# Kernel tuning notes

Hardware: AMD Instinct MI355X
Metric: run time of the kernel (lower is better)

Reference implementation:

```python
import jax, jax.numpy as jnp
import numpy as np

B, N, E = 4, 8192, 131072
NODE_F, EDGE_F, HID, ACT = 16, 1, 128, 8


def _glorot(key, shape):
    fan_in, fan_out = shape[0], shape[1]
    lim = np.sqrt(6.0 / (fan_in + fan_out))
    return jax.random.uniform(key, shape, jnp.float32, -lim, lim)


def setup_inputs() -> dict:
    key = jax.random.key(0)
    ks = jax.random.split(key, 20)
    inp = {
        'node_features': jax.random.randint(ks[0], (B, N, NODE_F), 0, 10, jnp.int32),
        'edge_index': jax.random.randint(ks[1], (B, 2, E), 0, N, jnp.int64),
        'edge_features': jax.random.normal(ks[2], (B, E, EDGE_F), jnp.float32),
        # conv1: in = 2*NODE_F + EDGE_F
        'c1_w1': _glorot(ks[3], (2 * NODE_F + EDGE_F, HID)), 'c1_b1': jnp.zeros((HID,), jnp.float32),
        'c1_w2': _glorot(ks[4], (HID, HID)), 'c1_b2': jnp.zeros((HID,), jnp.float32),
        # conv2/conv3: in = 2*HID + 1
        'c2_w1': _glorot(ks[5], (2 * HID + 1, HID)), 'c2_b1': jnp.zeros((HID,), jnp.float32),
        'c2_w2': _glorot(ks[6], (HID, HID)), 'c2_b2': jnp.zeros((HID,), jnp.float32),
        'c3_w1': _glorot(ks[7], (2 * HID + 1, HID)), 'c3_b1': jnp.zeros((HID,), jnp.float32),
        'c3_w2': _glorot(ks[8], (HID, HID)), 'c3_b2': jnp.zeros((HID,), jnp.float32),
        'lin_w': _glorot(ks[9], (NODE_F + HID, ACT)), 'lin_b': jnp.zeros((ACT,), jnp.float32),
    }
    return inp


def _edge_conv(x, src, dst, ea, w1, b1, w2, b2):
    # message: cat([x_i (target), x_j (source), edge_attr]) -> Linear -> LeakyReLU -> Linear
    m = jnp.concatenate([x[dst], x[src], ea], axis=1)          # [E, 2F+EF]
    m = jax.nn.leaky_relu(m @ w1 + b1) @ w2 + b2               # [E, out]
    out = jax.ops.segment_min(m, dst, num_segments=x.shape[0])  # min-aggregate at targets
    cnt = jnp.zeros((x.shape[0],), m.dtype).at[dst].add(1.0)
    return jnp.where(cnt[:, None] > 0, out, 0.0)                # nodes w/o in-edges -> 0 (PyG)


def _graph_fwd(x0, ei, ea, p):
    x0 = x0.astype(jnp.float32)  # torch casts to IntTensor then MLP promotes; math on integer values
    src, dst = ei[0], ei[1]      # flow='source_to_target'
    x = jax.nn.leaky_relu(_edge_conv(x0, src, dst, ea, p['c1_w1'], p['c1_b1'], p['c1_w2'], p['c1_b2']))
    x = jax.nn.leaky_relu(_edge_conv(x, src, dst, ea, p['c2_w1'], p['c2_b1'], p['c2_w2'], p['c2_b2']))
    x = jax.nn.leaky_relu(_edge_conv(x, src, dst, ea, p['c3_w1'], p['c3_b1'], p['c3_w2'], p['c3_b2']))
    x = jnp.concatenate([x0, x], axis=1)
    return jax.nn.softplus(x @ p['lin_w'] + p['lin_b'])         # [N, ACT]


def reference(node_features, edge_index, edge_features,
              c1_w1, c1_b1, c1_w2, c1_b2,
              c2_w1, c2_b1, c2_w2, c2_b2,
              c3_w1, c3_b1, c3_w2, c3_b2,
              lin_w, lin_b):
    p = dict(c1_w1=c1_w1, c1_b1=c1_b1, c1_w2=c1_w2, c1_b2=c1_b2,
             c2_w1=c2_w1, c2_b1=c2_b1, c2_w2=c2_w2, c2_b2=c2_b2,
             c3_w1=c3_w1, c3_b1=c3_b1, c3_w2=c3_w2, c3_b2=c3_b2,
             lin_w=lin_w, lin_b=lin_b)
    return jax.vmap(lambda x, ei, ea: _graph_fwd(x, ei, ea, p))(
        node_features, edge_index, edge_features)               # [B, N, ACT]
```

## Files before the change

### kernel.cpp

```cpp
#include <hip/hip_runtime.h>

#define B_ 4
#define N_ 8192
#define E_ 131072
#define HID_ 128

typedef unsigned short us8 __attribute__((ext_vector_type(8)));
typedef unsigned short us4 __attribute__((ext_vector_type(4)));
typedef unsigned int   ui4 __attribute__((ext_vector_type(4)));
typedef int            i4  __attribute__((ext_vector_type(4)));
typedef __bf16         v8bf __attribute__((ext_vector_type(8)));
typedef _Float16       hf8 __attribute__((ext_vector_type(8)));
typedef float          v4f  __attribute__((ext_vector_type(4)));
typedef float          v2f  __attribute__((ext_vector_type(2)));

#define KEY_INF 0xFF800000u

__device__ __forceinline__ float b2f(unsigned short u) {
    return __uint_as_float(((unsigned)u) << 16);
}
__device__ __forceinline__ unsigned short f2b(float f) {
    unsigned x = __float_as_uint(f);
    return (unsigned short)((x + 0x7fffu + ((x >> 16) & 1u)) >> 16);
}
__device__ __forceinline__ unsigned short f2h(float f) {
    union { _Float16 h; unsigned short u; } c; c.h = (_Float16)f; return c.u;
}
__device__ __forceinline__ unsigned fkey(float f) {
    unsigned b = __float_as_uint(f);
    return (b & 0x80000000u) ? ~b : (b | 0x80000000u);
}
__device__ __forceinline__ float funkey(unsigned k) {
    unsigned b = (k & 0x80000000u) ? (k ^ 0x80000000u) : ~k;
    return __uint_as_float(b);
}

__device__ __forceinline__ void repack_one(const float* __restrict__ w1, const float* __restrict__ w2,
                                           unsigned short* __restrict__ w1n, unsigned short* __restrict__ w2t,
                                           int F, int KPAD, int gid) {
    int t1 = 256 * KPAD;
    if (gid < t1) {
        int j = gid / KPAD, k = gid - j * KPAD;
        float v = 0.f;
        if (k < F) v = (j < 128) ? w1[k * 128 + j] : w1[(F + k) * 128 + (j - 128)];
        w1n[gid] = f2b(v);
    } else {
        int g = gid - t1;
        if (g < 16384) { int j = g >> 7, k = g & 127; w2t[g] = f2h(w2[k * 128 + j]); }
    }
}

__global__ void k_setup(const int* __restrict__ nf, unsigned short* __restrict__ x0b,
                        unsigned* __restrict__ cnt, unsigned* __restrict__ agg,
                        const float* __restrict__ w1a, const float* __restrict__ w2a,
                        const float* __restrict__ w1b, const float* __restrict__ w2b,
                        const float* __restrict__ w1c, const float* __restrict__ w2c,
                        unsigned short* __restrict__ w1n0, unsigned short* __restrict__ w2t0,
                        unsigned short* __restrict__ w1n1, unsigned short* __restrict__ w2t1,
                        unsigned short* __restrict__ w1n2, unsigned short* __restrict__ w2t2) {
    const int bid = blockIdx.x, tid = threadIdx.x;
    if (bid >= 4096) {
        const int rb = bid - 4096;
        const int gid = rb * 256 + tid;
        if (rb < 96)       repack_one(w1a, w2a, w1n0, w2t0, 16, 32, gid);
        else if (rb < 288) repack_one(w1b, w2b, w1n1, w2t1, 128, 128, gid - 96 * 256);
        else               repack_one(w1c, w2c, w1n2, w2t2, 128, 128, gid - 288 * 256);
        return;
    }
    const int gid = bid * 256 + tid;
    ui4 v = {KEY_INF, KEY_INF, KEY_INF, KEY_INF};
    ((ui4*)agg)[gid] = v;
    if (bid < 512) {
        i4 x = ((const i4*)nf)[gid];
        us4 o;
        o[0] = f2b((float)x[0]); o[1] = f2b((float)x[1]);
        o[2] = f2b((float)x[2]); o[3] = f2b((float)x[3]);
        ((us4*)x0b)[gid] = o;
    }
    if (bid < 128) cnt[gid] = 0u;
}

__global__ void k_hist(const int* __restrict__ ei, unsigned* __restrict__ cnt) {
    int gid = blockIdx.x * 256 + threadIdx.x;
    int b = gid >> 17, e = gid & (E_ - 1);
    int dst = ei[(b << 18) + E_ + e];
    atomicAdd(&cnt[(b << 13) + dst], 1u);
}

__global__ __launch_bounds__(1024) void k_scan(unsigned* __restrict__ cnt) {
    int b = blockIdx.x;
    __shared__ unsigned ps[1024];
    unsigned* c = cnt + (b << 13) + threadIdx.x * 8;
    unsigned loc[8]; unsigned s = 0;
#pragma unroll
    for (int i = 0; i < 8; i++) { loc[i] = c[i]; s += loc[i]; }
    ps[threadIdx.x] = s;
    __syncthreads();
    for (int off = 1; off < 1024; off <<= 1) {
        unsigned v = (threadIdx.x >= (unsigned)off) ? ps[threadIdx.x - off] : 0u;
        __syncthreads();
        ps[threadIdx.x] += v;
        __syncthreads();
    }
    unsigned run = ps[threadIdx.x] - s;
#pragma unroll
    for (int i = 0; i < 8; i++) { c[i] = run; run += loc[i]; }
}

template<int KPAD, bool FROM_AGG>
__device__ __forceinline__ void node_body(
    int bid,
    const unsigned short* __restrict__ xin,
    unsigned* __restrict__ agg,
    const unsigned short* __restrict__ w1n,
    const float* __restrict__ bias1,
    unsigned short* __restrict__ Yd,
    unsigned short* __restrict__ Ys,
    char* smem)
{
    constexpr int ASTR = KPAD + 8;
    unsigned short* A  = (unsigned short*)smem;
    unsigned short* Yb = (unsigned short*)(smem + 64 * ASTR * 2);

    const int tid = threadIdx.x;
    const int wave = tid >> 6, lane = tid & 63, lq = lane >> 4, lm = lane & 15;
    const int tile = (bid & 7) * 64 + (bid >> 3);
    const int n0 = tile * 64;

    v8bf wf[4][KPAD / 32]; float b1v[4];
#pragma unroll
    for (int nt = 0; nt < 4; nt++) {
        const int col = wave * 64 + nt * 16 + lm;
#pragma unroll
        for (int ks = 0; ks < KPAD / 32; ks++)
            wf[nt][ks] = *(const v8bf*)&w1n[col * KPAD + ks * 32 + lq * 8];
        b1v[nt] = (col < 128) ? bias1[col] : 0.f;
    }

    {
        const int row = tid >> 2, p = tid & 3;
        if (FROM_AGG) {
#pragma unroll
            for (int i = 0; i < 8; i++) {
                const int c = p + 4 * i;
                unsigned* ap = agg + ((size_t)(n0 + row)) * 128 + c * 4;
                ui4 k = *(ui4*)ap;
                ui4 inf = {KEY_INF, KEY_INF, KEY_INF, KEY_INF};
                *(ui4*)ap = inf;
                us4 o;
#pragma unroll
                for (int j = 0; j < 4; j++) {
                    float v = (k[j] == KEY_INF) ? 0.f : funkey(k[j]);
                    v = (v > 0.f) ? v : 0.01f * v;
                    o[j] = f2b(v);
                }
                *(us4*)&A[row * ASTR + c * 4] = o;
            }
        } else {
            us4 v = *(const us4*)(xin + ((size_t)(n0 + row)) * 16 + p * 4);
            *(us4*)&A[row * ASTR + p * 4] = v;
            us4 z = {0, 0, 0, 0};
            *(us4*)&A[row * ASTR + 16 + p * 4] = z;
        }
    }
    __syncthreads();

#pragma unroll
    for (int mt = 0; mt < 4; mt++) {
        v4f acc[4];
#pragma unroll
        for (int nt = 0; nt < 4; nt++) acc[nt] = v4f{0.f, 0.f, 0.f, 0.f};
#pragma unroll
        for (int ks = 0; ks < KPAD / 32; ks++) {
            v8bf a = *(const v8bf*)&A[(mt * 16 + lm) * ASTR + ks * 32 + lq * 8];
#pragma unroll
            for (int nt = 0; nt < 4; nt++)
                acc[nt] = __builtin_amdgcn_mfma_f32_16x16x32_bf16(a, wf[nt][ks], acc[nt], 0, 0, 0);
        }
#pragma unroll
        for (int nt = 0; nt < 4; nt++) {
            const int col = wave * 64 + nt * 16 + lm;
#pragma unroll
            for (int r = 0; r < 4; r++)
                Yb[(mt * 16 + lq * 4 + r) * 264 + col] = f2h(acc[nt][r] + b1v[nt]);
        }
    }
    __syncthreads();

    const int bb = tile >> 7, nl0 = (tile & 127) * 64;
#pragma unroll
    for (int i = 0; i < 8; i++) {
        const int idx = tid + 256 * i;
        const int row = idx >> 5, c = idx & 31;
        us8 v = *(const us8*)&Yb[row * 264 + c * 8];
        const int col0 = c * 8;
        unsigned short* dp = (col0 < 128)
            ? (Yd + ((size_t)(bb * N_) + nl0 + row) * 128 + col0)
            : (Ys + ((size_t)(bb * N_) + nl0 + row) * 128 + (col0 - 128));
        *(us8*)dp = v;
    }
}

template<int KPAD>
__global__ __launch_bounds__(256, 3) void k_node(
    const unsigned short* __restrict__ xin, unsigned* __restrict__ agg,
    const unsigned short* __restrict__ w1n, const float* __restrict__ bias1,
    unsigned short* __restrict__ Yd, unsigned short* __restrict__ Ys)
{
    __shared__ __align__(16) char smem[64 * (KPAD + 8) * 2 + 64 * 264 * 2];
    node_body<KPAD, true>(blockIdx.x, xin, agg, w1n, bias1, Yd, Ys, smem);
}

__global__ __launch_bounds__(256, 3) void k_scat_node1(
    const int* __restrict__ ei, unsigned* __restrict__ wptr, int* __restrict__ perm,
    const unsigned short* __restrict__ x0b,
    const unsigned short* __restrict__ w1n, const float* __restrict__ bias1,
    unsigned short* __restrict__ Yd, unsigned short* __restrict__ Ys)
{
    __shared__ __align__(16) char smem[64 * 40 * 2 + 64 * 264 * 2];
    const int bid = blockIdx.x;
    if (bid < 2048) {
        int gid = bid * 256 + threadIdx.x;
        int b = gid >> 17, e = gid & (E_ - 1);
        int dst = ei[(b << 18) + E_ + e];
        unsigned pos = atomicAdd(&wptr[(b << 13) + dst], 1u);
        perm[(b << 17) + pos] = e;
        return;
    }
    node_body<32, false>(bid - 2048, x0b, (unsigned*)nullptr, w1n, bias1, Yd, Ys, smem);
}

__global__ __launch_bounds__(256, 4) void k_edge(
    const unsigned short* __restrict__ Yd,
    const unsigned short* __restrict__ Ys,
    const int* __restrict__ ei,
    const float* __restrict__ eaf,
    const int* __restrict__ perm,
    const unsigned short* __restrict__ w2t,
    const float* __restrict__ weap,
    const float* __restrict__ bias2,
    unsigned* __restrict__ agg)
{
    __shared__ __align__(16) unsigned short Hs[2][64 * 128];
    __shared__ __align__(16) int      dstl[2][64];

    const int tid = threadIdx.x;
    const int wave = tid >> 6, lane = tid & 63, lq = lane >> 4, lm = lane & 15;

    hf8 w2f[2][4]; float b2v[2];
#pragma unroll
    for (int nt = 0; nt < 2; nt++) {
        const int col = wave * 32 + nt * 16 + lm;
#pragma unroll
        for (int ks = 0; ks < 4; ks++)
            w2f[nt][ks] = *(const hf8*)&w2t[col * 128 + ks * 32 + lq * 8];
        b2v[nt] = bias2[col];
    }

    const int arow = tid >> 2, p = tid & 3;
    const int lqg = (arow >> 2) & 3, mtg = arow >> 4, rg = arow & 3;
    const int sl  = lqg * 16 + mtg * 4 + rg;
    const int se0 = lqg * 128 + mtg * 4 + rg;
    const int rsw = arow & 15;

    hf8 wl0, wl1, wl2, wl3;
    {
        const float* wp = weap + p * 8;
#pragma unroll
        for (int u = 0; u < 8; u++) {
            wl0[u] = (_Float16)wp[u];
            wl1[u] = (_Float16)wp[32 + u];
            wl2[u] = (_Float16)wp[64 + u];
            wl3[u] = (_Float16)wp[96 + u];
        }
    }

    __syncthreads();

    const int chunk = (blockIdx.x & 7) * 128 + (blockIdx.x >> 3);
    const int b = chunk >> 8;
    const int ebase = (b << 17) + (chunk & 255) * 512;

    const hf8 c01v = {(_Float16)0.01f, (_Float16)0.01f, (_Float16)0.01f, (_Float16)0.01f,
                      (_Float16)0.01f, (_Float16)0.01f, (_Float16)0.01f, (_Float16)0.01f};

    int e   = perm[ebase + se0];
    int src = ei[(b << 18) + e];
    int dst = ei[(b << 18) + E_ + e];
    float ea = eaf[(b << 17) + e];

    {
        const hf8* ydp = (const hf8*)(Yd + ((size_t)(b * N_) + dst) * 128);
        const hf8* ysp = (const hf8*)(Ys + ((size_t)(b * N_) + src) * 128);
        if (p == 0) dstl[0][sl] = dst;
        const _Float16 eh = (_Float16)ea;
        const hf8 ea8 = {eh, eh, eh, eh, eh, eh, eh, eh};
        hf8 z;
        z = ydp[p] + ysp[p] + wl0 * ea8;
        z = __builtin_elementwise_max(z, z * c01v);
        *(hf8*)&Hs[0][arow * 128 + ((p ^ rsw) * 8)] = z;
        z = ydp[p + 4] + ysp[p + 4] + wl1 * ea8;
        z = __builtin_elementwise_max(z, z * c01v);
        *(hf8*)&Hs[0][arow * 128 + (((p + 4) ^ rsw) * 8)] = z;
        z = ydp[p + 8] + ysp[p + 8] + wl2 * ea8;
        z = __builtin_elementwise_max(z, z * c01v);
        *(hf8*)&Hs[0][arow * 128 + (((p + 8) ^ rsw) * 8)] = z;
        z = ydp[p + 12] + ysp[p + 12] + wl3 * ea8;
        z = __builtin_elementwise_max(z, z * c01v);
        *(hf8*)&Hs[0][arow * 128 + (((p + 12) ^ rsw) * 8)] = z;
    }
    __syncthreads();

    const int col0 = wave * 32 + lm, col1 = col0 + 16;
    unsigned* aggb = agg + (size_t)(b * N_) * 128;
    float cur0 = 0.f, cur1 = 0.f; int curd = -1; bool fseg = true;

    for (int jj = 0; jj < 8; jj++) {
        const int buf = jj & 1;

        if (jj < 7) {
            e   = perm[ebase + se0 + (jj + 1) * 16];
            src = ei[(b << 18) + e];
            dst = ei[(b << 18) + E_ + e];
            ea  = eaf[(b << 17) + e];
        }

        {
#pragma unroll
            for (int mt = 0; mt < 4; mt++) {
                const int row = mt * 16 + lm;
                v4f acc0 = {b2v[0], b2v[0], b2v[0], b2v[0]};
                v4f acc1 = {b2v[1], b2v[1], b2v[1], b2v[1]};
#pragma unroll
                for (int ks = 0; ks < 4; ks++) {
                    hf8 a = *(const hf8*)&Hs[buf][row * 128 + (((ks * 4 + lq) ^ lm) * 8)];
                    acc0 = __builtin_amdgcn_mfma_f32_16x16x32_f16(a, w2f[0][ks], acc0, 0, 0, 0);
                    acc1 = __builtin_amdgcn_mfma_f32_16x16x32_f16(a, w2f[1][ks], acc1, 0, 0, 0);
                }
                i4 dv = *(const i4*)&dstl[buf][lq * 16 + mt * 4];
#pragma unroll
                for (int r = 0; r < 4; r++) {
                    const float v0 = acc0[r];
                    const float v1 = acc1[r];
                    const int d = dv[r];
                    if (d != curd) {
                        if (curd >= 0) {
                            unsigned* p0 = aggb + (size_t)curd * 128 + col0;
                            unsigned* p1 = aggb + (size_t)curd * 128 + col1;
                            if (fseg) {
                                atomicMin(p0, fkey(cur0));
                                atomicMin(p1, fkey(cur1));
                            } else {
                                *p0 = fkey(cur0);
                                *p1 = fkey(cur1);
                            }
                            fseg = false;
                        }
                        curd = d; cur0 = v0; cur1 = v1;
                    } else {
                        cur0 = fminf(cur0, v0); cur1 = fminf(cur1, v1);
                    }
                }
            }
        }

        if (jj < 7) {
            const hf8* ydp = (const hf8*)(Yd + ((size_t)(b * N_) + dst) * 128);
            const hf8* ysp = (const hf8*)(Ys + ((size_t)(b * N_) + src) * 128);
            if (p == 0) dstl[buf ^ 1][sl] = dst;
            const _Float16 eh = (_Float16)ea;
            const hf8 ea8 = {eh, eh, eh, eh, eh, eh, eh, eh};
            hf8 z;
            z = ydp[p] + ysp[p] + wl0 * ea8;
            z = __builtin_elementwise_max(z, z * c01v);
            *(hf8*)&Hs[buf ^ 1][arow * 128 + ((p ^ rsw) * 8)] = z;
            z = ydp[p + 4] + ysp[p + 4] + wl1 * ea8;
            z = __builtin_elementwise_max(z, z * c01v);
            *(hf8*)&Hs[buf ^ 1][arow * 128 + (((p + 4) ^ rsw) * 8)] = z;
            z = ydp[p + 8] + ysp[p + 8] + wl2 * ea8;
            z = __builtin_elementwise_max(z, z * c01v);
            *(hf8*)&Hs[buf ^ 1][arow * 128 + (((p + 8) ^ rsw) * 8)] = z;
            z = ydp[p + 12] + ysp[p + 12] + wl3 * ea8;
            z = __builtin_elementwise_max(z, z * c01v);
            *(hf8*)&Hs[buf ^ 1][arow * 128 + (((p + 12) ^ rsw) * 8)] = z;
        }
        __syncthreads();
    }

    atomicMin(aggb + (size_t)curd * 128 + col0, fkey(cur0));
    atomicMin(aggb + (size_t)curd * 128 + col1, fkey(cur1));
}

__global__ __launch_bounds__(256, 4) void k_final(
    const unsigned short* __restrict__ x0b, const unsigned* __restrict__ agg,
    const float* __restrict__ lw, const float* __restrict__ lb,
    float* __restrict__ out) {
    __shared__ float w[144 * 8];
    __shared__ float bias8[8];
    __shared__ float xs[64 * 129];
    const int tid = threadIdx.x;
    for (int i = tid; i < 1152; i += 256) w[i] = lw[i];
    if (tid < 8) bias8[tid] = lb[tid];
    const int n0 = blockIdx.x * 64;
#pragma unroll
    for (int i = 0; i < 8; i++) {
        const int idx = tid + 256 * i;
        const int row = idx >> 5, c = idx & 31;
        ui4 k = ((const ui4*)(agg + ((size_t)(n0 + row)) * 128))[c];
#pragma unroll
        for (int j = 0; j < 4; j++) {
            float v = (k[j] == KEY_INF) ? 0.f : funkey(k[j]);
            v = fmaxf(v, 0.01f * v);
            xs[row * 129 + c * 4 + j] = v;
        }
    }
    __syncthreads();
    const int node = tid >> 2, ap = (tid & 3) * 2;
    float a0 = bias8[ap], a1 = bias8[ap + 1];
    const unsigned short* x0 = x0b + (size_t)(n0 + node) * 16;
#pragma unroll
    for (int f = 0; f < 16; f++) {
        const float xv = b2f(x0[f]);
        a0 += xv * w[f * 8 + ap]; a1 += xv * w[f * 8 + ap + 1];
    }
    const float* xr = &xs[node * 129];
#pragma unroll 8
    for (int f = 0; f < 128; f++) {
        const float xv = xr[f];
        a0 += xv * w[(16 + f) * 8 + ap]; a1 += xv * w[(16 + f) * 8 + ap + 1];
    }
    v2f o;
    o[0] = fmaxf(a0, 0.f) + log1pf(expf(-fabsf(a0)));
    o[1] = fmaxf(a1, 0.f) + log1pf(expf(-fabsf(a1)));
    *(v2f*)&out[(size_t)(n0 + node) * 8 + ap] = o;
}

extern "C" void kernel_launch(void* const* d_in, const int* in_sizes, int n_in,
                              void* d_out, int out_size, void* d_ws, size_t ws_size,
                              hipStream_t stream) {
    (void)in_sizes; (void)n_in; (void)out_size; (void)ws_size;
    const int* nf  = (const int*)d_in[0];
    const int* ei  = (const int*)d_in[1];
    const float* eaf = (const float*)d_in[2];
    const float* cw1[3] = {(const float*)d_in[3],  (const float*)d_in[7],  (const float*)d_in[11]};
    const float* cb1[3] = {(const float*)d_in[4],  (const float*)d_in[8],  (const float*)d_in[12]};
    const float* cw2[3] = {(const float*)d_in[5],  (const float*)d_in[9],  (const float*)d_in[13]};
    const float* cb2[3] = {(const float*)d_in[6],  (const float*)d_in[10], (const float*)d_in[14]};
    const float* lw = (const float*)d_in[15];
    const float* lb = (const float*)d_in[16];
    float* out = (float*)d_out;

    size_t off = 0;
    auto carve = [&](size_t bytes) { void* p = (char*)d_ws + off; off += (bytes + 255) & ~(size_t)255; return p; };
    unsigned short* x0b  = (unsigned short*)carve((size_t)B_ * N_ * 16 * 2);
    unsigned*       agg  = (unsigned*)carve((size_t)B_ * N_ * 128 * 4);
    unsigned*       cnt  = (unsigned*)carve((size_t)B_ * N_ * 4);
    int*            perm = (int*)carve((size_t)B_ * E_ * 4);
    unsigned short* Yd   = (unsigned short*)carve((size_t)B_ * N_ * 128 * 2);
    unsigned short* Ys   = (unsigned short*)carve((size_t)B_ * N_ * 128 * 2);
    unsigned short* w1n0 = (unsigned short*)carve(256 * 32 * 2);
    unsigned short* w2t0 = (unsigned short*)carve(128 * 128 * 2);
    unsigned short* w1n1 = (unsigned short*)carve(256 * 128 * 2);
    unsigned short* w2t1 = (unsigned short*)carve(128 * 128 * 2);
    unsigned short* w1n2 = (unsigned short*)carve(256 * 128 * 2);
    unsigned short* w2t2 = (unsigned short*)carve(128 * 128 * 2);

    k_setup<<<4576, 256, 0, stream>>>(nf, x0b, cnt, agg,
                                      cw1[0], cw2[0], cw1[1], cw2[1], cw1[2], cw2[2],
                                      w1n0, w2t0, w1n1, w2t1, w1n2, w2t2);
    k_hist<<<2048, 256, 0, stream>>>(ei, cnt);
    k_scan<<<B_, 1024, 0, stream>>>(cnt);

    k_scat_node1<<<2560, 256, 0, stream>>>(ei, cnt, perm, x0b, w1n0, cb1[0], Yd, Ys);
    k_edge<<<1024, 256, 0, stream>>>(Yd, Ys, ei, eaf, perm, w2t0, cw1[0] + 32 * 128, cb2[0], agg);

    k_node<128><<<512, 256, 0, stream>>>(x0b, agg, w1n1, cb1[1], Yd, Ys);
    k_edge<<<1024, 256, 0, stream>>>(Yd, Ys, ei, eaf, perm, w2t1, cw1[1] + 256 * 128, cb2[1], agg);

    k_node<128><<<512, 256, 0, stream>>>(x0b, agg, w1n2, cb1[2], Yd, Ys);
    k_edge<<<1024, 256, 0, stream>>>(Yd, Ys, ei, eaf, perm, w2t2, cw1[2] + 256 * 128, cb2[2], agg);

    k_final<<<512, 256, 0, stream>>>(x0b, agg, lw, lb, out);
}
```

Before: 289.1 us.

## Fuse destination histogram and prefix scan into setup kernel using LDS atomics

Removes the separate global-atomic histogram and scan kernels. Instead, four extra blocks appended to the setup kernel each build one batch's in-degree histogram in shared memory, then run a wave-shuffle exclusive scan that writes offsets straight to the count buffer. This saves two launches and the global atomics, but one 256-thread block must now process all 131072 edges of a batch, which may leave a long serial tail. The 32KB static LDS allocation also applies to every setup block and could lower occupancy.

```diff
diff --git a/kernel.cpp b/kernel.cpp
--- a/kernel.cpp
+++ b/kernel.cpp
@@ -52,13 +52,59 @@
 
 __global__ void k_setup(const int* __restrict__ nf, unsigned short* __restrict__ x0b,
                         unsigned* __restrict__ cnt, unsigned* __restrict__ agg,
+                        const int* __restrict__ ei,
                         const float* __restrict__ w1a, const float* __restrict__ w2a,
                         const float* __restrict__ w1b, const float* __restrict__ w2b,
                         const float* __restrict__ w1c, const float* __restrict__ w2c,
                         unsigned short* __restrict__ w1n0, unsigned short* __restrict__ w2t0,
                         unsigned short* __restrict__ w1n1, unsigned short* __restrict__ w2t1,
                         unsigned short* __restrict__ w1n2, unsigned short* __restrict__ w2t2) {
+    __shared__ unsigned hsh[8192];
+    __shared__ unsigned hsw[4];
     const int bid = blockIdx.x, tid = threadIdx.x;
+    if (bid >= 4576) {
+        const int hb = bid - 4576;
+        for (int i = tid; i < 8192; i += 256) hsh[i] = 0u;
+        __syncthreads();
+        const i4* dp = (const i4*)(ei + (hb << 18) + E_);
+#pragma unroll 8
+        for (int k = 0; k < 128; k++) {
+            i4 d = dp[k * 256 + tid];
+            atomicAdd(&hsh[d[0]], 1u); atomicAdd(&hsh[d[1]], 1u);
+            atomicAdd(&hsh[d[2]], 1u); atomicAdd(&hsh[d[3]], 1u);
+        }
+        __syncthreads();
+        unsigned loc[32]; unsigned s = 0;
+#pragma unroll
+        for (int i = 0; i < 8; i++) {
+            ui4 v = *(ui4*)&hsh[tid * 32 + i * 4];
+            loc[i * 4] = v[0]; loc[i * 4 + 1] = v[1];
+            loc[i * 4 + 2] = v[2]; loc[i * 4 + 3] = v[3];
+            s += v[0] + v[1] + v[2] + v[3];
+        }
+        unsigned incl = s;
+#pragma unroll
+        for (int off = 1; off < 64; off <<= 1) {
+            unsigned v = __shfl_up(incl, off);
+            if ((tid & 63) >= (unsigned)off) incl += v;
+        }
+        if ((tid & 63) == 63) hsw[tid >> 6] = incl;
+        __syncthreads();
+        unsigned wp = 0;
+        for (int w = 0; w < (tid >> 6); w++) wp += hsw[w];
+        unsigned run = wp + incl - s;
+        unsigned* c = cnt + (hb << 13) + tid * 32;
+#pragma unroll
+        for (int i = 0; i < 8; i++) {
+            ui4 o;
+            o[0] = run; run += loc[i * 4];
+            o[1] = run; run += loc[i * 4 + 1];
+            o[2] = run; run += loc[i * 4 + 2];
+            o[3] = run; run += loc[i * 4 + 3];
+            *(ui4*)&c[i * 4] = o;
+        }
+        return;
+    }
     if (bid >= 4096) {
         const int rb = bid - 4096;
         const int gid = rb * 256 + tid;
@@ -77,34 +123,6 @@
         o[2] = f2b((float)x[2]); o[3] = f2b((float)x[3]);
         ((us4*)x0b)[gid] = o;
     }
-    if (bid < 128) cnt[gid] = 0u;
-}
-
-__global__ void k_hist(const int* __restrict__ ei, unsigned* __restrict__ cnt) {
-    int gid = blockIdx.x * 256 + threadIdx.x;
-    int b = gid >> 17, e = gid & (E_ - 1);
-    int dst = ei[(b << 18) + E_ + e];
-    atomicAdd(&cnt[(b << 13) + dst], 1u);
-}
-
-__global__ __launch_bounds__(1024) void k_scan(unsigned* __restrict__ cnt) {
-    int b = blockIdx.x;
-    __shared__ unsigned ps[1024];
-    unsigned* c = cnt + (b << 13) + threadIdx.x * 8;
-    unsigned loc[8]; unsigned s = 0;
-#pragma unroll
-    for (int i = 0; i < 8; i++) { loc[i] = c[i]; s += loc[i]; }
-    ps[threadIdx.x] = s;
-    __syncthreads();
-    for (int off = 1; off < 1024; off <<= 1) {
-        unsigned v = (threadIdx.x >= (unsigned)off) ? ps[threadIdx.x - off] : 0u;
-        __syncthreads();
-        ps[threadIdx.x] += v;
-        __syncthreads();
-    }
-    unsigned run = ps[threadIdx.x] - s;
-#pragma unroll
-    for (int i = 0; i < 8; i++) { c[i] = run; run += loc[i]; }
 }
 
 template<int KPAD, bool FROM_AGG>
@@ -465,11 +483,9 @@
     unsigned short* w1n2 = (unsigned short*)carve(256 * 128 * 2);
     unsigned short* w2t2 = (unsigned short*)carve(128 * 128 * 2);
 
-    k_setup<<<4576, 256, 0, stream>>>(nf, x0b, cnt, agg,
+    k_setup<<<4580, 256, 0, stream>>>(nf, x0b, cnt, agg, ei,
                                       cw1[0], cw2[0], cw1[1], cw2[1], cw1[2], cw2[2],
                                       w1n0, w2t0, w1n1, w2t1, w1n2, w2t2);
-    k_hist<<<2048, 256, 0, stream>>>(ei, cnt);
-    k_scan<<<B_, 1024, 0, stream>>>(cnt);
 
     k_scat_node1<<<2560, 256, 0, stream>>>(ei, cnt, perm, x0b, w1n0, cb1[0], Yd, Ys);
     k_edge<<<1024, 256, 0, stream>>>(Yd, Ys, ei, eaf, perm, w2t0, cw1[0] + 32 * 128, cb2[0], agg);
```

Result: slower. 302.7 us (+4.7%).
